# Performance work log

Measured on AMD Instinct MI355X. Metric: run time of the kernel, lower is better.

Reference implementation:

```python
import jax, jax.numpy as jnp
import numpy as np

N_ATOMS = 8388608
N_MOLS = 262144


def setup_inputs() -> dict:
    key = jax.random.key(0)
    k1, k2, k3 = jax.random.split(key, 3)
    # h[:,0] = e (electronegativity), h[:,1] = s (hardness, must be > 0)
    h = jax.random.uniform(k1, (N_ATOMS, 2), dtype=jnp.float32)
    h = h.at[:, 1].add(0.5)  # keep hardness away from zero (1/s used)
    q = jax.random.normal(k2, (N_ATOMS,), dtype=jnp.float32)
    mol_id = jnp.sort(jax.random.randint(k3, (N_ATOMS,), 0, N_MOLS, dtype=jnp.int64))
    return {"h": h, "q": q, "mol_id": mol_id, "n_mols": N_MOLS}


def reference(h, q, mol_id, n_mols):
    """Charge equilibrium via Lagrange multipliers.

    q_i* = -e_i/s_i + (1/s_i) * (Q + sum_j e_j/s_j) / (sum_j 1/s_j)
    where sums run over atoms of the same molecule and Q = sum_j q_j.
    """
    e = h[:, 0]
    s = h[:, 1]
    s_inv = 1.0 / s
    e_s_inv = e * s_inv
    # atom -> mol segment sums (atom_in_mol), then mol -> atom broadcast (mol_has_atom)
    sum_q = jax.ops.segment_sum(q, mol_id, num_segments=n_mols)[mol_id]
    sum_s_inv = jax.ops.segment_sum(s_inv, mol_id, num_segments=n_mols)[mol_id]
    sum_e_s_inv = jax.ops.segment_sum(e_s_inv, mol_id, num_segments=n_mols)[mol_id]
    q_hat = -e * s_inv + s_inv * (sum_q + sum_e_s_inv) / sum_s_inv
    return q_hat
```

## Files before the change

### kernel.cpp

```cpp
#include <hip/hip_runtime.h>

#define N_ATOMS 8388608
#define N_MOLS  262144
#define N_PAIRS (N_ATOMS / 2)
#define TPB     256
#define PPB     512
#define APB     1024
#define NBLK    (N_PAIRS / PPB)
#define NBOUND  (NBLK - 1)
#define BINS    1280

template<int CTRL, int RM>
__device__ __forceinline__ int dpp_key(int v) {
    return __builtin_amdgcn_update_dpp(-1, v, CTRL, RM, 0xf, false);
}
template<int CTRL, int RM>
__device__ __forceinline__ float dpp_val(float v) {
    return __int_as_float(
        __builtin_amdgcn_update_dpp(0, __float_as_int(v), CTRL, RM, 0xf, false));
}

__global__ __launch_bounds__(TPB) void ce_main(
    const float4* __restrict__ h4, const float2* __restrict__ q2,
    const int2* __restrict__ mol2, float2* __restrict__ out2,
    int* __restrict__ headKey, float2* __restrict__ headVal,
    int* __restrict__ headEnd,
    int* __restrict__ tailKey, float2* __restrict__ tailVal,
    int* __restrict__ tailStart, int* __restrict__ flags)
{
    __shared__ float bq[BINS], bs[BINS];
    __shared__ int sFirst, sLast, sHeadEnd, sTailStart;

    const int t = threadIdx.x;
    const int lane = t & 63;
    const int B = blockIdx.x;
    const int pbase = B * PPB;
    const int p0 = pbase + t, p1 = pbase + TPB + t;

    float4 h0 = h4[p0], h1 = h4[p1];
    float2 q0 = q2[p0], q1 = q2[p1];
    int2   m0 = mol2[p0], m1 = mol2[p1];

    for (int i = t; i < BINS; i += TPB) { bq[i] = 0.f; bs[i] = 0.f; }
    if (t == 0) { sFirst = m0.x; sHeadEnd = -1; sTailStart = 0x7fffffff; }
    if (t == TPB - 1) sLast = m1.y;
    __syncthreads();
    const int mF = sFirst, mL = sLast;
    const bool bad = (mL - mF >= BINS);

    float si00, esi00, si01, esi01, si10, esi10, si11, esi11;

#define CHUNK(hv, qv, mv, PIDX, SI0, ESI0, SI1, ESI1)                        \
    {                                                                        \
        float si0 = 1.0f / hv.y, si1 = 1.0f / hv.w;                          \
        float esi0 = hv.x * si0, esi1 = hv.z * si1;                          \
        float qe0 = qv.x + esi0, qe1 = qv.y + esi1;                          \
        bool  b = (mv.x != mv.y);                                            \
        int   key = mv.y;                                                    \
        float pq = b ? qe1 : (qe0 + qe1);                                    \
        float ps = b ? si1 : (si0 + si1);                                    \
        if (b) {                                                             \
            int idx = min(mv.x - mF, BINS - 1);                              \
            atomicAdd(&bq[idx], qe0); atomicAdd(&bs[idx], si0);              \
        }                                                                    \
        SCAN_STEP(0x111, 0xf) SCAN_STEP(0x112, 0xf)                          \
        SCAN_STEP(0x114, 0xf) SCAN_STEP(0x118, 0xf)                          \
        SCAN_STEP(0x142, 0xa) SCAN_STEP(0x143, 0xc)                          \
        int  nk = __shfl_down(key, 1, 64);                                   \
        bool tail = (lane == 63) || (nk != key);                             \
        if (tail) {                                                          \
            int idx = min(key - mF, BINS - 1);                               \
            atomicAdd(&bq[idx], pq); atomicAdd(&bs[idx], ps);                \
        }                                                                    \
        int a0 = (PIDX) * 2;                                                 \
        if (mv.y == mF)      atomicMax(&sHeadEnd, a0 + 1);                   \
        else if (mv.x == mF) atomicMax(&sHeadEnd, a0);                       \
        if (mv.x == mL)      atomicMin(&sTailStart, a0);                     \
        else if (mv.y == mL) atomicMin(&sTailStart, a0 + 1);                 \
        SI0 = si0; ESI0 = esi0; SI1 = si1; ESI1 = esi1;                      \
    }
#define SCAN_STEP(CTRL, RM)                                                  \
    {                                                                        \
        int   k  = dpp_key<CTRL, RM>(key);                                   \
        float vq = dpp_val<CTRL, RM>(pq);                                    \
        float vs = dpp_val<CTRL, RM>(ps);                                    \
        if (k == key) { pq += vq; ps += vs; }                                \
    }

    CHUNK(h0, q0, m0, p0, si00, esi00, si01, esi01)
    CHUNK(h1, q1, m1, p1, si10, esi10, si11, esi11)
#undef SCAN_STEP
#undef CHUNK

    __syncthreads();
    if (t == 0) {
        headKey[B] = mF;
        headVal[B] = make_float2(bq[0], bs[0]);
        headEnd[B] = sHeadEnd;
        flags[B]   = bad ? 1 : 0;
    }
    if (t == 64) {
        int li = min(mL - mF, BINS - 1);
        tailKey[B]   = mL;
        tailVal[B]   = make_float2(bq[li], bs[li]);
        tailStart[B] = sTailStart;
    }
    __syncthreads();
    for (int i = t; i < BINS; i += TPB) bq[i] = bq[i] / bs[i];
    __syncthreads();

    int i00 = min(m0.x - mF, BINS - 1), i01 = min(m0.y - mF, BINS - 1);
    int i10 = min(m1.x - mF, BINS - 1), i11 = min(m1.y - mF, BINS - 1);
    out2[p0] = make_float2(bq[i00] * si00 - esi00, bq[i01] * si01 - esi01);
    out2[p1] = make_float2(bq[i10] * si10 - esi10, bq[i11] * si11 - esi11);
}

__global__ __launch_bounds__(TPB) void ce_cleanup(
    const float2* __restrict__ h2, float* __restrict__ out,
    const int* __restrict__ headKey, const float2* __restrict__ headVal,
    const int* __restrict__ headEnd,
    const int* __restrict__ tailKey, const float2* __restrict__ tailVal,
    const int* __restrict__ tailStart)
{
    int i = blockIdx.x * 4 + (threadIdx.x >> 6);
    if (i >= NBOUND) return;
    int lane = threadIdx.x & 63;

    int M = tailKey[i];
    if (headKey[i + 1] != M) return;
    if (headKey[i] == M && i > 0 && tailKey[i - 1] == M) return;

    float2 tot = tailVal[i];
    int start = tailStart[i];
    int j = i + 1;
    float2 hv1 = headVal[j];
    tot.x += hv1.x; tot.y += hv1.y;
    while (j < NBOUND && tailKey[j] == M && headKey[j + 1] == M) {
        ++j;
        float2 hvj = headVal[j];
        tot.x += hvj.x; tot.y += hvj.y;
    }
    int end = headEnd[j];
    float tt = tot.x / tot.y;
    for (int a = start + lane; a <= end; a += 64) {
        float2 hv = h2[a];
        out[a] = (tt - hv.x) / hv.y;
    }
}

__global__ __launch_bounds__(TPB) void ce_repair(
    const float2* __restrict__ h2, const float* __restrict__ q,
    const int* __restrict__ mol, float* __restrict__ out,
    const int* __restrict__ flags)
{
    for (int fb = blockIdx.x * 32; fb < blockIdx.x * 32 + 32; ++fb) {
        if (!flags[fb]) continue;
        int bStart = fb * APB;
        if (threadIdx.x == 0) {
            int s = bStart;
            while (s > 0 && mol[s - 1] == mol[bStart]) --s;
            if (s < bStart) {
                int m = mol[s];
                float sq = 0.f, ss = 0.f; int e = s;
                for (int x = s; x < N_ATOMS && mol[x] == m; ++x) {
                    float2 hv = h2[x]; float si = 1.0f / hv.y;
                    sq += q[x] + hv.x * si; ss += si; e = x;
                }
                float tt = sq / ss;
                for (int x = s; x <= e; ++x) {
                    float2 hv = h2[x]; out[x] = (tt - hv.x) / hv.y;
                }
            }
        }
        for (int a = bStart + threadIdx.x; a < bStart + APB; a += TPB) {
            if (a != 0 && mol[a - 1] == mol[a]) continue;
            int m = mol[a];
            float sq = 0.f, ss = 0.f; int e = a;
            for (int x = a; x < N_ATOMS && mol[x] == m; ++x) {
                float2 hv = h2[x]; float si = 1.0f / hv.y;
                sq += q[x] + hv.x * si; ss += si; e = x;
            }
            float tt = sq / ss;
            for (int x = a; x <= e; ++x) {
                float2 hv = h2[x]; out[x] = (tt - hv.x) / hv.y;
            }
        }
    }
}

extern "C" void kernel_launch(void* const* d_in, const int* in_sizes, int n_in,
                              void* d_out, int out_size, void* d_ws, size_t ws_size,
                              hipStream_t stream) {
    const float4* h4   = (const float4*)d_in[0];
    const float2* h2   = (const float2*)d_in[0];
    const float*  q    = (const float*)d_in[1];
    const float2* q2   = (const float2*)d_in[1];
    const int*    mol  = (const int*)d_in[2];
    const int2*   mol2 = (const int2*)d_in[2];
    float2* out2 = (float2*)d_out;
    float*  out  = (float*)d_out;

    float2* headVal   = (float2*)d_ws;
    float2* tailVal   = headVal + NBLK;
    int*    headKey   = (int*)(tailVal + NBLK);
    int*    tailKey   = headKey + NBLK;
    int*    headEnd   = tailKey + NBLK;
    int*    tailStart = headEnd + NBLK;
    int*    flags     = tailStart + NBLK;

    ce_main<<<NBLK, TPB, 0, stream>>>(h4, q2, mol2, out2,
                                      headKey, headVal, headEnd,
                                      tailKey, tailVal, tailStart, flags);
    ce_cleanup<<<(NBOUND + 3) / 4, TPB, 0, stream>>>(h2, out,
                                                     headKey, headVal, headEnd,
                                                     tailKey, tailVal, tailStart);
    ce_repair<<<NBLK / 32, TPB, 0, stream>>>(h2, q, mol, out, flags);
}
```

Measured before the change: 38.73 us.

## Shrink shared bins and fuse boundary cleanup with overflow repair kernel

Reduces the per-block shared histogram from 1280 to 192 bins, so init and normalise become a single guarded step and LDS use drops, which may raise occupancy. Merges the boundary-chain cleanup and the overflow repair into one kernel, saving a launch. Chains that touch a flagged block are skipped so the repair path owns them. Risk: with fewer bins more blocks overflow and fall back to the slow serial repair path.

```diff
diff --git a/kernel.cpp b/kernel.cpp
--- a/kernel.cpp
+++ b/kernel.cpp
@@ -8,7 +8,7 @@
 #define APB     1024
 #define NBLK    (N_PAIRS / PPB)
 #define NBOUND  (NBLK - 1)
-#define BINS    1280
+#define BINS    192
 
 template<int CTRL, int RM>
 __device__ __forceinline__ int dpp_key(int v) {
@@ -41,7 +41,7 @@
     float2 q0 = q2[p0], q1 = q2[p1];
     int2   m0 = mol2[p0], m1 = mol2[p1];
 
-    for (int i = t; i < BINS; i += TPB) { bq[i] = 0.f; bs[i] = 0.f; }
+    if (t < BINS) { bq[t] = 0.f; bs[t] = 0.f; }
     if (t == 0) { sFirst = m0.x; sHeadEnd = -1; sTailStart = 0x7fffffff; }
     if (t == TPB - 1) sLast = m1.y;
     __syncthreads();
@@ -106,7 +106,7 @@
         tailStart[B] = sTailStart;
     }
     __syncthreads();
-    for (int i = t; i < BINS; i += TPB) bq[i] = bq[i] / bs[i];
+    if (t < BINS) bq[t] = bq[t] / bs[t];
     __syncthreads();
 
     int i00 = min(m0.x - mF, BINS - 1), i01 = min(m0.y - mF, BINS - 1);
@@ -115,45 +115,48 @@
     out2[p1] = make_float2(bq[i10] * si10 - esi10, bq[i11] * si11 - esi11);
 }
 
-__global__ __launch_bounds__(TPB) void ce_cleanup(
-    const float2* __restrict__ h2, float* __restrict__ out,
+__global__ __launch_bounds__(TPB) void ce_fixup(
+    const float2* __restrict__ h2, const float* __restrict__ q,
+    const int* __restrict__ mol, float* __restrict__ out,
     const int* __restrict__ headKey, const float2* __restrict__ headVal,
     const int* __restrict__ headEnd,
     const int* __restrict__ tailKey, const float2* __restrict__ tailVal,
-    const int* __restrict__ tailStart)
+    const int* __restrict__ tailStart, const int* __restrict__ flags)
 {
-    int i = blockIdx.x * 4 + (threadIdx.x >> 6);
-    if (i >= NBOUND) return;
-    int lane = threadIdx.x & 63;
-
-    int M = tailKey[i];
-    if (headKey[i + 1] != M) return;
-    if (headKey[i] == M && i > 0 && tailKey[i - 1] == M) return;
-
-    float2 tot = tailVal[i];
-    int start = tailStart[i];
-    int j = i + 1;
-    float2 hv1 = headVal[j];
-    tot.x += hv1.x; tot.y += hv1.y;
-    while (j < NBOUND && tailKey[j] == M && headKey[j + 1] == M) {
-        ++j;
-        float2 hvj = headVal[j];
-        tot.x += hvj.x; tot.y += hvj.y;
-    }
-    int end = headEnd[j];
-    float tt = tot.x / tot.y;
-    for (int a = start + lane; a <= end; a += 64) {
-        float2 hv = h2[a];
-        out[a] = (tt - hv.x) / hv.y;
-    }
-}
-
-__global__ __launch_bounds__(TPB) void ce_repair(
-    const float2* __restrict__ h2, const float* __restrict__ q,
-    const int* __restrict__ mol, float* __restrict__ out,
-    const int* __restrict__ flags)
-{
-    for (int fb = blockIdx.x * 32; fb < blockIdx.x * 32 + 32; ++fb) {
+    {
+        int i = blockIdx.x * 4 + (threadIdx.x >> 6);
+        int lane = threadIdx.x & 63;
+        if (i < NBOUND) {
+            int M = tailKey[i];
+            bool skip = flags[i] || flags[i + 1];
+            if (!skip && headKey[i + 1] == M &&
+                !(headKey[i] == M && i > 0 && tailKey[i - 1] == M)) {
+                float2 tot = tailVal[i];
+                int start = tailStart[i];
+                int j = i + 1;
+                float2 hv1 = headVal[j];
+                tot.x += hv1.x; tot.y += hv1.y;
+                bool chainBad = false;
+                while (j < NBOUND && tailKey[j] == M && headKey[j + 1] == M) {
+                    ++j;
+                    if (flags[j]) chainBad = true;
+                    float2 hvj = headVal[j];
+                    tot.x += hvj.x; tot.y += hvj.y;
+                }
+                if (j < NBLK && flags[j]) chainBad = true;
+                if (!chainBad) {
+                    int end = headEnd[j];
+                    float tt = tot.x / tot.y;
+                    for (int a = start + lane; a <= end; a += 64) {
+                        float2 hv = h2[a];
+                        out[a] = (tt - hv.x) / hv.y;
+                    }
+                }
+            }
+        }
+    }
+
+    for (int fb = blockIdx.x * 4; fb < blockIdx.x * 4 + 4 && fb < NBLK; ++fb) {
         if (!flags[fb]) continue;
         int bStart = fb * APB;
         if (threadIdx.x == 0) {
@@ -211,8 +214,8 @@
     ce_main<<<NBLK, TPB, 0, stream>>>(h4, q2, mol2, out2,
                                       headKey, headVal, headEnd,
                                       tailKey, tailVal, tailStart, flags);
-    ce_cleanup<<<(NBOUND + 3) / 4, TPB, 0, stream>>>(h2, out,
-                                                     headKey, headVal, headEnd,
-                                                     tailKey, tailVal, tailStart);
-    ce_repair<<<NBLK / 32, TPB, 0, stream>>>(h2, q, mol, out, flags);
-}
+    ce_fixup<<<(NBOUND + 3) / 4, TPB, 0, stream>>>(h2, q, mol, out,
+                                                   headKey, headVal, headEnd,
+                                                   tailKey, tailVal, tailStart,
+                                                   flags);
+}
```

Result: faster. 36.71 us (-5.2%).
